# Kernel tuning notes

Measured on AMD Instinct MI355X. Metric: run time of the kernel, lower is better.

Reference implementation:

```python
import jax, jax.numpy as jnp
import numpy as np

B, N, C = 8, 4096, 512
NUM_HEADS = 8
HEAD_DIM = C // NUM_HEADS
POS_RES = 32  # only table with res <= max_resolution=32


def _interp_linear(pos, out_len):
    # F.interpolate(mode='linear', align_corners=False) along the length axis (axis 1)
    in_len = pos.shape[1]
    scale = in_len / out_len
    coords = (jnp.arange(out_len, dtype=jnp.float32) + 0.5) * scale - 0.5
    coords = jnp.clip(coords, 0.0, in_len - 1)
    i0 = jnp.floor(coords).astype(jnp.int32)
    i1 = jnp.minimum(i0 + 1, in_len - 1)
    w = (coords - i0.astype(jnp.float32))[None, :, None]
    return pos[:, i0, :] * (1.0 - w) + pos[:, i1, :] * w


def setup_inputs():
    key = jax.random.key(0)
    k = jax.random.split(key, 4)
    x = jax.random.normal(k[0], (B, N, C), jnp.float32)
    pos_32 = jax.random.normal(k[1], (1, POS_RES ** 3, C), jnp.float32)  # torch.randn init
    s = 1.0 / np.sqrt(C)
    w_qkv = jax.random.normal(k[2], (C, 3 * C), jnp.float32) * s
    b_qkv = jnp.zeros((3 * C,), jnp.float32)
    w_proj = jax.random.normal(k[3], (C, C), jnp.float32) * s
    b_proj = jnp.zeros((C,), jnp.float32)
    return {"x": x, "pos_32": pos_32, "w_qkv": w_qkv, "b_qkv": b_qkv,
            "w_proj": w_proj, "b_proj": b_proj, "resolution": 16}


def reference(x, pos_32, w_qkv, b_qkv, w_proj, b_proj, resolution):
    Bx, Nx, Cx = x.shape
    target_len = resolution ** 3  # 4096 -> nearest table pos_32 is interpolated down
    pos = pos_32 if pos_32.shape[1] == target_len else _interp_linear(pos_32, target_len)
    if pos.shape[1] == Nx:
        x = x + pos
    qkv = (x @ w_qkv + b_qkv).reshape(Bx, Nx, 3, NUM_HEADS, HEAD_DIM)
    q, k, v = qkv[:, :, 0], qkv[:, :, 1], qkv[:, :, 2]  # each [B, N, H, D]
    # Faithful to source: q,k,v are NOT permuted to [B,H,N,D], so q @ k.T
    # contracts head_dim per token, yielding [B, N, H, H] head-axis attention.
    attn = jnp.einsum('bnid,bnjd->bnij', q, k) / np.sqrt(HEAD_DIM)
    attn = jax.nn.softmax(attn, axis=-1)
    out = jnp.einsum('bnij,bnjd->bnid', attn, v)  # [B, N, H, D]
    # torch: .transpose(1, 2).reshape(B, N, C) -> flatten of [B, H, N, D]
    out = jnp.transpose(out, (0, 2, 1, 3)).reshape(Bx, Nx, Cx)
    return out @ w_proj + b_proj
```

## Files before the change

kernel.cpp:

```cpp
#include <hip/hip_runtime.h>
#include <hip/hip_bf16.h>

using bf16 = __hip_bfloat16;
typedef __attribute__((ext_vector_type(8))) short short8;
typedef __attribute__((ext_vector_type(4))) float f32x4;

#define AS1U(p) ((const __attribute__((address_space(1))) unsigned int*)(p))
#define AS3U(p) ((__attribute__((address_space(3))) unsigned int*)(p))

__device__ __forceinline__ float bflo(unsigned u) { return __uint_as_float(u << 16); }
__device__ __forceinline__ float bfhi(unsigned u) { return __uint_as_float(u & 0xffff0000u); }
__device__ __forceinline__ unsigned short f2bf(float f) {
    union { float f; unsigned u; } v{f};
    unsigned r = v.u + 0x7fffu + ((v.u >> 16) & 1u);
    return (unsigned short)(r >> 16);
}

__global__ __launch_bounds__(256) void kprep(const float* __restrict__ wq,
                                             const float* __restrict__ wp,
                                             const float* __restrict__ x,
                                             const float* __restrict__ pos,
                                             bf16* __restrict__ wqT,
                                             bf16* __restrict__ wpT,
                                             bf16* __restrict__ xp) {
    int bid = blockIdx.x;
    __shared__ float t[32][33];
    if (bid < 1024) {
        const float* in; bf16* out; int Cc, bx, by;
        if (bid < 768) { in = wq; out = wqT; Cc = 1536; bx = bid % 48; by = bid / 48; }
        else { int i = bid - 768; in = wp; out = wpT; Cc = 512; bx = i & 15; by = i >> 4; }
        const int R = 512;
        int tx = threadIdx.x & 31, ty = threadIdx.x >> 5;
        int c0 = bx * 32, r0 = by * 32;
#pragma unroll
        for (int i = 0; i < 4; ++i)
            t[ty + i * 8][tx] = in[(size_t)(r0 + ty + i * 8) * Cc + c0 + tx];
        __syncthreads();
#pragma unroll
        for (int i = 0; i < 4; ++i)
            out[(size_t)(c0 + ty + i * 8) * R + r0 + tx] = __float2bfloat16(t[tx][ty + i * 8]);
    } else {
        size_t idx4 = (size_t)(bid - 1024) * 256 + threadIdx.x;
        size_t e = idx4 * 4;
        int c = (int)(e & 511);
        size_t m = e >> 9;
        int n = (int)(m & 4095);
        float4 xv = *(const float4*)(x + e);
        float4 p3 = *(const float4*)(pos + (size_t)(n * 8 + 3) * 512 + c);
        float4 p4 = *(const float4*)(pos + (size_t)(n * 8 + 4) * 512 + c);
        unsigned r[2];
        float v0 = xv.x + 0.5f * (p3.x + p4.x);
        float v1 = xv.y + 0.5f * (p3.y + p4.y);
        float v2 = xv.z + 0.5f * (p3.z + p4.z);
        float v3 = xv.w + 0.5f * (p3.w + p4.w);
        r[0] = (unsigned)f2bf(v0) | ((unsigned)f2bf(v1) << 16);
        r[1] = (unsigned)f2bf(v2) | ((unsigned)f2bf(v3) << 16);
        *(uint2*)(xp + e) = *(uint2*)r;
    }
}

template <typename OutT>
__global__ __launch_bounds__(512, 2) void kgemm8(const bf16* __restrict__ A,
                                                 const bf16* __restrict__ Bt,
                                                 const float* __restrict__ bias,
                                                 OutT* __restrict__ C,
                                                 int M, int N, int K) {
    __shared__ __align__(16) char smem[131072];
    const int tid = threadIdx.x;
    const int lane = tid & 63, wave = tid >> 6;
    const int wm = wave >> 2, wn = wave & 3;
    const int fr = lane & 15;
    const int g = lane >> 4;
    const int s0 = ((g ^ (fr & 7)) << 4);
    const int s1 = (((g | 4) ^ (fr & 7)) << 4);

    const int ntn = N >> 8;
    const int nwg = gridDim.x;
    const int bid = blockIdx.x;
    const int swz = (bid & 7) * (nwg >> 3) + (bid >> 3);
    const int bm = (swz / ntn) << 8;
    const int bn = (swz % ntn) << 8;

    const int r = wave * 8 + (lane >> 3);
    const int o = ((lane & 7) ^ ((lane >> 3) & 7)) * 8;
    const bf16* srcA[4]; const bf16* srcB[4];
#pragma unroll
    for (int h = 0; h < 2; ++h)
#pragma unroll
        for (int jj = 0; jj < 2; ++jj) {
            srcA[h * 2 + jj] = A  + (size_t)(bm + h * 128 + jj * 64 + r) * K + o;
            srcB[h * 2 + jj] = Bt + (size_t)(bn + h * 128 + jj * 64 + r) * K + o;
        }

    const char* pA0[2]; const char* pA1[2]; const char* pB0[2]; const char* pB1[2];
#pragma unroll
    for (int b = 0; b < 2; ++b) {
        const char* abase = smem + b * 65536 + wm * 16384 + fr * 128;
        const char* bbase = smem + b * 65536 + 32768 + (wn >> 1) * 16384 + (wn & 1) * 8192 + fr * 128;
        pA0[b] = abase + s0; pA1[b] = abase + s1;
        pB0[b] = bbase + s0; pB1[b] = bbase + s1;
    }

    f32x4 acc[8][4];
#pragma unroll
    for (int i = 0; i < 8; ++i)
#pragma unroll
        for (int j = 0; j < 4; ++j) acc[i][j] = f32x4{0.f, 0.f, 0.f, 0.f};

    auto stage = [&](int kt, int b) {
        char* base = smem + b * 65536;
#pragma unroll
        for (int i = 0; i < 4; ++i) {
            const int off = (i >> 1) * 16384 + (i & 1) * 8192 + wave * 1024;
            __builtin_amdgcn_global_load_lds(AS1U(srcA[i] + kt * 64), AS3U(base + off), 16, 0, 0);
            __builtin_amdgcn_global_load_lds(AS1U(srcB[i] + kt * 64), AS3U(base + 32768 + off), 16, 0, 0);
        }
    };

    stage(0, 0);
    stage(1, 1);

#pragma unroll
    for (int t = 0; t < 8; ++t) {
        const int b = t & 1;
        if (t < 7) asm volatile("s_waitcnt vmcnt(8)" ::: "memory");
        else       asm volatile("s_waitcnt vmcnt(0)" ::: "memory");
        __builtin_amdgcn_s_barrier();
        __builtin_amdgcn_sched_barrier(0);
#pragma unroll
        for (int kk = 0; kk < 2; ++kk) {
            const char* pA = kk ? pA1[b] : pA0[b];
            const char* pB = kk ? pB1[b] : pB0[b];
            short8 af[8];
#pragma unroll
            for (int mi = 0; mi < 8; ++mi)
                af[mi] = *(const short8*)(pA + mi * 2048);
#pragma unroll
            for (int njh = 0; njh < 2; ++njh) {
                short8 bfr[2];
#pragma unroll
                for (int j = 0; j < 2; ++j)
                    bfr[j] = *(const short8*)(pB + (njh * 2 + j) * 2048);
                __builtin_amdgcn_s_setprio(1);
#pragma unroll
                for (int mi = 0; mi < 8; ++mi)
#pragma unroll
                    for (int j = 0; j < 2; ++j)
                        acc[mi][njh * 2 + j] = __builtin_amdgcn_mfma_f32_16x16x32_bf16(
                            af[mi], bfr[j], acc[mi][njh * 2 + j], 0, 0, 0);
                __builtin_amdgcn_s_setprio(0);
            }
        }
        __builtin_amdgcn_sched_barrier(0);
        __builtin_amdgcn_s_barrier();
        if (t < 6) stage(t + 2, b);
    }

#pragma unroll
    for (int mi = 0; mi < 8; ++mi) {
#pragma unroll
        for (int nj = 0; nj < 4; ++nj) {
            int col = bn + wn * 64 + nj * 16 + fr;
            int row0 = bm + wm * 128 + mi * 16 + (lane >> 4) * 4;
            float bv = bias[col];
#pragma unroll
            for (int rr = 0; rr < 4; ++rr) {
                float val = acc[mi][nj][rr] + bv;
                if constexpr (sizeof(OutT) == 2)
                    C[(size_t)(row0 + rr) * N + col] = (OutT)__float2bfloat16(val);
                else
                    C[(size_t)(row0 + rr) * N + col] = (OutT)val;
            }
        }
    }
}

__global__ __launch_bounds__(256) void kattn(const bf16* __restrict__ qkv,
                                             bf16* __restrict__ oscr) {
    int T = blockIdx.x * 256 + threadIdx.x;
    int token = T >> 3, head = T & 7;
    int b = token >> 12, n = token & 4095;
    const bf16* row = qkv + (size_t)token * 1536;

    uint4 qp[8];
#pragma unroll
    for (int c = 0; c < 8; ++c) qp[c] = *(const uint4*)(row + head * 64 + c * 8);

    float s[8];
#pragma unroll
    for (int j = 0; j < 8; ++j) {
        float acc = 0.f;
#pragma unroll
        for (int c = 0; c < 8; ++c) {
            uint4 kp = *(const uint4*)(row + 512 + j * 64 + c * 8);
            const unsigned* ku = &kp.x; const unsigned* qu = &qp[c].x;
#pragma unroll
            for (int w = 0; w < 4; ++w) {
                acc = fmaf(bflo(qu[w]), bflo(ku[w]), acc);
                acc = fmaf(bfhi(qu[w]), bfhi(ku[w]), acc);
            }
        }
        s[j] = acc * 0.125f;
    }
    float mx = s[0];
#pragma unroll
    for (int j = 1; j < 8; ++j) mx = fmaxf(mx, s[j]);
    float sum = 0.f;
#pragma unroll
    for (int j = 0; j < 8; ++j) { s[j] = __expf(s[j] - mx); sum += s[j]; }
    float inv = 1.f / sum;
#pragma unroll
    for (int j = 0; j < 8; ++j) s[j] *= inv;

    float o[64];
#pragma unroll
    for (int d = 0; d < 64; ++d) o[d] = 0.f;
#pragma unroll
    for (int j = 0; j < 8; ++j) {
        float pj = s[j];
#pragma unroll
        for (int c = 0; c < 8; ++c) {
            uint4 vp = *(const uint4*)(row + 1024 + j * 64 + c * 8);
            const unsigned* vu = &vp.x;
#pragma unroll
            for (int w = 0; w < 4; ++w) {
                o[c * 8 + w * 2]     = fmaf(pj, bflo(vu[w]), o[c * 8 + w * 2]);
                o[c * 8 + w * 2 + 1] = fmaf(pj, bfhi(vu[w]), o[c * 8 + w * 2 + 1]);
            }
        }
    }
    size_t orow = (size_t)b * 4096 + head * 512 + (n >> 3);
    bf16* op = oscr + orow * 512 + (n & 7) * 64;
#pragma unroll
    for (int c = 0; c < 8; ++c) {
        unsigned rr[4];
#pragma unroll
        for (int w = 0; w < 4; ++w)
            rr[w] = (unsigned)f2bf(o[c * 8 + w * 2]) | ((unsigned)f2bf(o[c * 8 + w * 2 + 1]) << 16);
        *(uint4*)(op + c * 8) = *(uint4*)rr;
    }
}

extern "C" void kernel_launch(void* const* d_in, const int* in_sizes, int n_in,
                              void* d_out, int out_size, void* d_ws, size_t ws_size,
                              hipStream_t stream) {
    const float* x      = (const float*)d_in[0];
    const float* pos32  = (const float*)d_in[1];
    const float* w_qkv  = (const float*)d_in[2];
    const float* b_qkv  = (const float*)d_in[3];
    const float* w_proj = (const float*)d_in[4];
    const float* b_proj = (const float*)d_in[5];

    char* ws = (char*)d_ws;
    bf16* xp   = (bf16*)(ws);
    bf16* qkv  = (bf16*)(ws + 33554432);
    bf16* wqT  = (bf16*)(ws + 134217728);
    bf16* wpT  = (bf16*)(ws + 135790592);
    bf16* ascr = xp;

    kprep<<<17408, 256, 0, stream>>>(w_qkv, w_proj, x, pos32, wqT, wpT, xp);
    kgemm8<bf16><<<768, 512, 0, stream>>>(xp, wqT, b_qkv, qkv, 32768, 1536, 512);
    kattn<<<1024, 256, 0, stream>>>(qkv, ascr);
    kgemm8<float><<<256, 512, 0, stream>>>(ascr, wpT, b_proj, (float*)d_out, 32768, 512, 512);
}
```

Measured before the change: 146.8 us.

## Restructure GEMM mainloop into 4-slot K=32 pipeline with interleaved staging

Replaces the double-buffered K=64 tile loop with a four-slot ring of K=32 tiles, prefetching three stages ahead. A and B loads are issued separately between two MFMA half-phases, with a new LDS swizzle and row mapping. K is also fixed at compile time as 512. The aim is to hide global-to-LDS latency better and spread memory issue across the compute. The cost is more barriers per K step and a kernel hardcoded to K=512.

New measurement: 144.0 us. No clear change (-1.9%).

```diff
diff --git a/kernel.cpp b/kernel.cpp
--- a/kernel.cpp
+++ b/kernel.cpp
@@ -64,15 +64,18 @@
                                                  const bf16* __restrict__ Bt,
                                                  const float* __restrict__ bias,
                                                  OutT* __restrict__ C,
-                                                 int M, int N, int K) {
+                                                 int M, int N, int K_) {
+    constexpr int K = 512;
     __shared__ __align__(16) char smem[131072];
     const int tid = threadIdx.x;
     const int lane = tid & 63, wave = tid >> 6;
     const int wm = wave >> 2, wn = wave & 3;
     const int fr = lane & 15;
     const int g = lane >> 4;
-    const int s0 = ((g ^ (fr & 7)) << 4);
-    const int s1 = (((g | 4) ^ (fr & 7)) << 4);
+
+    const int p_rd = (((fr & 1) << 2) | g) ^ ((fr >> 1) & 7);
+    const int tbA = (wm * 64 + (fr >> 1)) * 128 + p_rd * 16;
+    const int tbB = (wn * 32 + (fr >> 1)) * 128 + p_rd * 16;
 
     const int ntn = N >> 8;
     const int nwg = gridDim.x;
@@ -81,25 +84,16 @@
     const int bm = (swz / ntn) << 8;
     const int bn = (swz % ntn) << 8;
 
-    const int r = wave * 8 + (lane >> 3);
-    const int o = ((lane & 7) ^ ((lane >> 3) & 7)) * 8;
-    const bf16* srcA[4]; const bf16* srcB[4];
-#pragma unroll
-    for (int h = 0; h < 2; ++h)
-#pragma unroll
-        for (int jj = 0; jj < 2; ++jj) {
-            srcA[h * 2 + jj] = A  + (size_t)(bm + h * 128 + jj * 64 + r) * K + o;
-            srcB[h * 2 + jj] = Bt + (size_t)(bn + h * 128 + jj * 64 + r) * K + o;
-        }
-
-    const char* pA0[2]; const char* pA1[2]; const char* pB0[2]; const char* pB1[2];
-#pragma unroll
-    for (int b = 0; b < 2; ++b) {
-        const char* abase = smem + b * 65536 + wm * 16384 + fr * 128;
-        const char* bbase = smem + b * 65536 + 32768 + (wn >> 1) * 16384 + (wn & 1) * 8192 + fr * 128;
-        pA0[b] = abase + s0; pA1[b] = abase + s1;
-        pB0[b] = bbase + s0; pB1[b] = bbase + s1;
-    }
+    const int q = (lane & 7) ^ (lane >> 3);
+    const int srow = wave * 32 + 2 * (lane >> 3) + ((q >> 2) & 1);
+    const int scol = (q & 3) * 8;
+    const bf16* sA[2]; const bf16* sB[2];
+#pragma unroll
+    for (int g2 = 0; g2 < 2; ++g2) {
+        sA[g2] = A  + (size_t)(bm + srow + g2 * 16) * K + scol;
+        sB[g2] = Bt + (size_t)(bn + srow + g2 * 16) * K + scol;
+    }
+    const int dA0 = wave * 2048, dA1 = wave * 2048 + 1024;
 
     f32x4 acc[8][4];
 #pragma unroll
@@ -107,53 +101,62 @@
 #pragma unroll
         for (int j = 0; j < 4; ++j) acc[i][j] = f32x4{0.f, 0.f, 0.f, 0.f};
 
-    auto stage = [&](int kt, int b) {
-        char* base = smem + b * 65536;
-#pragma unroll
-        for (int i = 0; i < 4; ++i) {
-            const int off = (i >> 1) * 16384 + (i & 1) * 8192 + wave * 1024;
-            __builtin_amdgcn_global_load_lds(AS1U(srcA[i] + kt * 64), AS3U(base + off), 16, 0, 0);
-            __builtin_amdgcn_global_load_lds(AS1U(srcB[i] + kt * 64), AS3U(base + 32768 + off), 16, 0, 0);
-        }
+    auto stageA = [&](int kt, int slot) {
+        char* d = smem + slot * 32768;
+        __builtin_amdgcn_global_load_lds(AS1U(sA[0] + kt * 32), AS3U(d + dA0), 16, 0, 0);
+        __builtin_amdgcn_global_load_lds(AS1U(sA[1] + kt * 32), AS3U(d + dA1), 16, 0, 0);
     };
-
-    stage(0, 0);
-    stage(1, 1);
-
-#pragma unroll
-    for (int t = 0; t < 8; ++t) {
-        const int b = t & 1;
-        if (t < 7) asm volatile("s_waitcnt vmcnt(8)" ::: "memory");
-        else       asm volatile("s_waitcnt vmcnt(0)" ::: "memory");
-        __builtin_amdgcn_s_barrier();
+    auto stageB = [&](int kt, int slot) {
+        char* d = smem + slot * 32768 + 16384;
+        __builtin_amdgcn_global_load_lds(AS1U(sB[0] + kt * 32), AS3U(d + dA0), 16, 0, 0);
+        __builtin_amdgcn_global_load_lds(AS1U(sB[1] + kt * 32), AS3U(d + dA1), 16, 0, 0);
+    };
+
+    stageA(0, 0); stageB(0, 0);
+    stageA(1, 1); stageB(1, 1);
+    stageA(2, 2); stageB(2, 2);
+    asm volatile("s_waitcnt vmcnt(8)" ::: "memory");
+    __builtin_amdgcn_s_barrier();
+
+#pragma unroll
+    for (int t = 0; t < 16; ++t) {
+        const int r = t & 3, rs = (t + 3) & 3;
+        const char* pa = smem + r * 32768;
+        const char* pb = pa + 16384;
+        short8 af0[4], bfr[4], af1[4];
+#pragma unroll
+        for (int mi = 0; mi < 4; ++mi) af0[mi] = *(const short8*)(pa + tbA + mi * 1024);
+#pragma unroll
+        for (int nj = 0; nj < 4; ++nj) bfr[nj] = *(const short8*)(pb + tbB + nj * 1024);
+        if (t < 13) stageA(t + 3, rs);
+        __builtin_amdgcn_s_barrier();
+        asm volatile("s_waitcnt lgkmcnt(0)" ::: "memory");
         __builtin_amdgcn_sched_barrier(0);
-#pragma unroll
-        for (int kk = 0; kk < 2; ++kk) {
-            const char* pA = kk ? pA1[b] : pA0[b];
-            const char* pB = kk ? pB1[b] : pB0[b];
-            short8 af[8];
-#pragma unroll
-            for (int mi = 0; mi < 8; ++mi)
-                af[mi] = *(const short8*)(pA + mi * 2048);
-#pragma unroll
-            for (int njh = 0; njh < 2; ++njh) {
-                short8 bfr[2];
-#pragma unroll
-                for (int j = 0; j < 2; ++j)
-                    bfr[j] = *(const short8*)(pB + (njh * 2 + j) * 2048);
-                __builtin_amdgcn_s_setprio(1);
-#pragma unroll
-                for (int mi = 0; mi < 8; ++mi)
-#pragma unroll
-                    for (int j = 0; j < 2; ++j)
-                        acc[mi][njh * 2 + j] = __builtin_amdgcn_mfma_f32_16x16x32_bf16(
-                            af[mi], bfr[j], acc[mi][njh * 2 + j], 0, 0, 0);
-                __builtin_amdgcn_s_setprio(0);
-            }
-        }
+        __builtin_amdgcn_s_setprio(1);
+#pragma unroll
+        for (int mi = 0; mi < 4; ++mi)
+#pragma unroll
+            for (int nj = 0; nj < 4; ++nj)
+                acc[mi][nj] = __builtin_amdgcn_mfma_f32_16x16x32_bf16(af0[mi], bfr[nj], acc[mi][nj], 0, 0, 0);
+        __builtin_amdgcn_s_setprio(0);
+        __builtin_amdgcn_s_barrier();
+#pragma unroll
+        for (int mi = 0; mi < 4; ++mi) af1[mi] = *(const short8*)(pa + tbA + (mi + 4) * 1024);
+        if (t < 13) stageB(t + 3, rs);
+        __builtin_amdgcn_s_barrier();
+        asm volatile("s_waitcnt lgkmcnt(0)" ::: "memory");
         __builtin_amdgcn_sched_barrier(0);
-        __builtin_amdgcn_s_barrier();
-        if (t < 6) stage(t + 2, b);
+        __builtin_amdgcn_s_setprio(1);
+#pragma unroll
+        for (int mi = 0; mi < 4; ++mi)
+#pragma unroll
+            for (int nj = 0; nj < 4; ++nj)
+                acc[mi + 4][nj] = __builtin_amdgcn_mfma_f32_16x16x32_bf16(af1[mi], bfr[nj], acc[mi + 4][nj], 0, 0, 0);
+        __builtin_amdgcn_s_setprio(0);
+        if (t <= 12)      asm volatile("s_waitcnt vmcnt(8)" ::: "memory");
+        else if (t == 13) asm volatile("s_waitcnt vmcnt(4)" ::: "memory");
+        else if (t == 14) asm volatile("s_waitcnt vmcnt(0)" ::: "memory");
+        __builtin_amdgcn_s_barrier();
     }
 
 #pragma unroll
```
